# Kernel tuning notes

Measured on AMD Instinct MI355X. Metric: run time of the kernel, lower is better.

Reference implementation:

```python
import jax, jax.numpy as jnp
import numpy as np

N_NODES = 50000
N_EDGES = 800000
IN_F = 128
HID = 256
N_CLS = 10
NUM_GRAPHS = 256


def setup_inputs() -> dict:
    key = jax.random.key(0)
    ks = jax.random.split(key, 8)
    x = jax.random.normal(ks[0], (N_NODES, IN_F), dtype=jnp.float32)
    edge_index = jax.random.randint(ks[1], (2, N_EDGES), 0, N_NODES, dtype=jnp.int64)
    batch = jnp.sort(jax.random.randint(ks[2], (N_NODES,), 0, NUM_GRAPHS, dtype=jnp.int64))
    # Glorot-style init for weights (GCNConv default), zeros bias
    W1 = jax.random.normal(ks[3], (IN_F, HID), dtype=jnp.float32) / np.sqrt(IN_F)
    b1 = jnp.zeros((HID,), dtype=jnp.float32)
    W2 = jax.random.normal(ks[4], (HID, HID), dtype=jnp.float32) / np.sqrt(HID)
    b2 = jnp.zeros((HID,), dtype=jnp.float32)
    Wlin = jax.random.normal(ks[5], (HID, N_CLS), dtype=jnp.float32) / np.sqrt(HID)
    blin = jnp.zeros((N_CLS,), dtype=jnp.float32)
    return {"x": x, "edge_index": edge_index, "batch": batch,
            "W1": W1, "b1": b1, "W2": W2, "b2": b2, "Wlin": Wlin, "blin": blin}


def reference(x, edge_index, batch, W1, b1, W2, b2, Wlin, blin):
    N = x.shape[0]
    # PyG GCNConv default: add self-loops, symmetric normalization D^-1/2 A D^-1/2
    loop = jnp.arange(N, dtype=edge_index.dtype)
    src = jnp.concatenate([edge_index[0], loop])  # message source (row)
    dst = jnp.concatenate([edge_index[1], loop])  # aggregation target (col)
    deg = jax.ops.segment_sum(jnp.ones_like(dst, dtype=x.dtype), dst, num_segments=N)
    dinv = jnp.where(deg > 0, jax.lax.rsqrt(deg), 0.0)
    norm = dinv[src] * dinv[dst]  # [E+N]

    def gcn_conv(h, W, b):
        h = h @ W                          # linear transform first (GCNConv)
        msg = h[src] * norm[:, None]       # gather + edge scale
        agg = jax.ops.segment_sum(msg, dst, num_segments=N)  # scatter-add
        return agg + b

    h = jax.nn.relu(gcn_conv(x, W1, b1))
    h = gcn_conv(h, W2, b2)

    # global_mean_pool over batch ids
    counts = jax.ops.segment_sum(jnp.ones((N,), x.dtype), batch, num_segments=NUM_GRAPHS)
    pooled = jax.ops.segment_sum(h, batch, num_segments=NUM_GRAPHS)
    pooled = pooled / jnp.maximum(counts, 1.0)[:, None]  # [NUM_GRAPHS, HID]

    return pooled @ Wlin + blin  # forward returns logits (softmax unused in forward)
```

## Files before the change

### kernel.cpp

```cpp
#include <hip/hip_runtime.h>
#include <hip/hip_bf16.h>

typedef __hip_bfloat16 bf16;
typedef __attribute__((ext_vector_type(8))) short short8;
typedef __attribute__((ext_vector_type(4))) float f32x4;
typedef __attribute__((ext_vector_type(2))) float f32x2;

#define N_NODES 50000
#define N_EDGES 800000
#define IN_F    128
#define HID     256
#define N_CLS   10
#define N_GRAPH 256

#define NB 98
#define PBLOCKS 256

__device__ __forceinline__ int IG(const int* __restrict__ p, int i, int w) {
    return w ? p[2 * i] : p[i];
}
__device__ __forceinline__ float LF(const void* __restrict__ p, int i, int isbf) {
    return isbf ? __bfloat162float(((const bf16*)p)[i]) : ((const float*)p)[i];
}
__device__ __forceinline__ float b2f(unsigned short h) {
    union { unsigned u; float f; } c; c.u = ((unsigned)h) << 16; return c.f;
}
__device__ __forceinline__ unsigned short f2b(float x) {
    bf16 h = __float2bfloat16(x);
    union { bf16 b; unsigned short u; } c; c.b = h; return c.u;
}
__device__ __forceinline__ float f8s(unsigned b) {
    union { unsigned u; float f; } c;
    c.u = ((b & 0x80u) << 24) | ((b & 0x7Fu) << 20);
    return c.f;
}
#define F8SCALE 0x1p120f
__device__ __forceinline__ unsigned f2fp8(float x) {
    unsigned short h = f2b(x * 0x1p-120f);
    unsigned s = ((unsigned)h >> 8) & 0x80u;
    unsigned mag = (unsigned)h & 0x7FFFu;
    unsigned r = (mag + 7u + ((mag >> 4) & 1u)) >> 4;
    if (r > 0x7Eu) r = 0x7Eu;
    return s | r;
}

#if defined(__has_builtin)
#if __has_builtin(__builtin_amdgcn_cvt_pk_f32_fp8)
#define HW_FP8 1
#endif
#if __has_builtin(__builtin_amdgcn_cvt_pk_fp8_f32)
#define HW_FP8E 1
#endif
#endif

__device__ __forceinline__ f32x2 cvt2lo(unsigned v) {
#ifdef HW_FP8
    return __builtin_amdgcn_cvt_pk_f32_fp8((int)v, false);
#else
    f32x2 r; r[0] = f8s(v & 0xFF) * F8SCALE; r[1] = f8s((v >> 8) & 0xFF) * F8SCALE; return r;
#endif
}
__device__ __forceinline__ f32x2 cvt2hi(unsigned v) {
#ifdef HW_FP8
    return __builtin_amdgcn_cvt_pk_f32_fp8((int)v, true);
#else
    f32x2 r; r[0] = f8s((v >> 16) & 0xFF) * F8SCALE; r[1] = f8s(v >> 24) * F8SCALE; return r;
#endif
}
__device__ __forceinline__ unsigned pk4_fp8(float v0, float v1, float v2, float v3) {
#ifdef HW_FP8E
    int o = __builtin_amdgcn_cvt_pk_fp8_f32(v0, v1, 0, false);
    o = __builtin_amdgcn_cvt_pk_fp8_f32(v2, v3, o, true);
    return (unsigned)o;
#else
    return f2fp8(v0) | (f2fp8(v1) << 8) | (f2fp8(v2) << 16) | (f2fp8(v3) << 24);
#endif
}

__global__ __launch_bounds__(256) void k_partA1(const int* __restrict__ ei, int* __restrict__ bucketCnt,
                                                int* __restrict__ blockBase,
                                                const unsigned short* __restrict__ x,
                                                int* __restrict__ flags, int E, int N) {
    int t = threadIdx.x;
    if (blockIdx.x == PBLOCKS) {
        __shared__ int nz, cnt;
        if (t == 0) { nz = 0; cnt = 0; }
        __syncthreads();
        int found = 0, c = 0;
        for (int s = 0; s < 4; ++s) {
            int idx = 2 * (t * 4 + s) + 1;
            if (ei[idx] != 0) found = 1;
        }
        for (int s = 0; s < 8; ++s) {
            unsigned short h = x[t * 8 + s];
            int e = (h >> 7) & 0xFF;
            if (e >= 110 && e <= 135) c++;
        }
        if (found) atomicAdd(&nz, 1);
        atomicAdd(&cnt, c);
        __syncthreads();
        if (t == 0) {
            flags[0] = (nz == 0) ? 1 : 0;
            flags[1] = (cnt > 1536) ? 1 : 0;
        }
        return;
    }
    __shared__ int h[NB];
    __shared__ int wsh;
    if (t == 0) wsh = 0;
    if (t < NB) h[t] = 0;
    __syncthreads();
    int found = 0;
    for (int s = 0; s < 4; ++s) {
        int idx = 2 * (t * 4 + s) + 1;
        if (ei[idx] != 0) found = 1;
    }
    if (found) atomicAdd(&wsh, 1);
    __syncthreads();
    int w = (wsh == 0) ? 1 : 0;
    for (int e = blockIdx.x * 256 + t; e < E; e += PBLOCKS * 256) {
        int d = IG(ei, E + e, w);
        int s = IG(ei, e, w);
        if ((unsigned)d < (unsigned)N && (unsigned)s < (unsigned)N)
            atomicAdd(&h[d >> 9], 1);
    }
    __syncthreads();
    if (t < NB)
        blockBase[blockIdx.x * NB + t] = atomicAdd(&bucketCnt[t * 16], h[t]);
}

__global__ __launch_bounds__(128) void k_bscan(const int* __restrict__ bucketCnt,
                                               int* __restrict__ bucketBase) {
    __shared__ int s[128];
    int t = threadIdx.x;
    int v = (t < NB) ? bucketCnt[t * 16] : 0;
    s[t] = v;
    __syncthreads();
    for (int off = 1; off < 128; off <<= 1) {
        int add = (t >= off) ? s[t - off] : 0;
        __syncthreads();
        s[t] += add;
        __syncthreads();
    }
    if (t <= NB) bucketBase[t] = (t < NB) ? (s[t] - v) : s[NB - 1] + 0;
    if (t == NB - 1) bucketBase[NB] = s[t];
}

__global__ __launch_bounds__(256) void k_partA2(const int* __restrict__ ei,
                                                const int* __restrict__ bucketBase,
                                                const int* __restrict__ blockBase,
                                                unsigned* __restrict__ part,
                                                const int* __restrict__ flags, int E, int N) {
    __shared__ int cur[NB];
    int t = threadIdx.x;
    if (t < NB) cur[t] = bucketBase[t] + blockBase[blockIdx.x * NB + t];
    __syncthreads();
    int w = flags[0];
    for (int e = blockIdx.x * 256 + t; e < E; e += PBLOCKS * 256) {
        int d = IG(ei, E + e, w);
        int s = IG(ei, e, w);
        if ((unsigned)d < (unsigned)N && (unsigned)s < (unsigned)N) {
            int slot = atomicAdd(&cur[d >> 9], 1);
            part[slot] = ((unsigned)(d & 511) << 16) | (unsigned)s;
        }
    }
}

#define PB_W1 98
#define PB_W2 226
#define PB_GB 482
#define PB_TOT 678
__global__ __launch_bounds__(256) void k_partB(const unsigned* __restrict__ part,
                                               const int* __restrict__ bucketBase,
                                               int* __restrict__ rowptr, float* __restrict__ dinv,
                                               int* __restrict__ col,
                                               const void* __restrict__ W1, unsigned short* __restrict__ w1t,
                                               const void* __restrict__ W2, unsigned short* __restrict__ w2t,
                                               const int* __restrict__ batch, int* __restrict__ gstart,
                                               const int* __restrict__ flags, int N) {
    int b = blockIdx.x, t = threadIdx.x;
    if (b >= NB) {
        int fb = flags[1];
        if (b < PB_W2) {
            int i = (b - PB_W1) * 256 + t;
            int n = i >> 7, k = i & 127;
            w1t[i] = f2b(LF(W1, k * 256 + n, fb));
        } else if (b < PB_GB) {
            int i = (b - PB_W2) * 256 + t;
            int n = i >> 8, k = i & 255;
            w2t[i] = f2b(LF(W2, k * 256 + n, fb));
        } else {
            int i = (b - PB_GB) * 256 + t;
            if (i <= N_NODES) {
                int w = flags[0];
                int prev = (i == 0) ? -1 : IG(batch, i - 1, w);
                int cur  = (i == N_NODES) ? N_GRAPH : IG(batch, i, w);
                if (prev < -1) prev = -1;
                if (cur > N_GRAPH) cur = N_GRAPH;
                for (int g = prev + 1; g <= cur; ++g)
                    if (g >= 0 && g <= N_GRAPH) gstart[g] = i;
            }
        }
        return;
    }
    __shared__ int hist[512];
    __shared__ int scn[512];
    __shared__ int pair[256];
    int s0 = bucketBase[b], e0 = bucketBase[b + 1];
    hist[t] = 0; hist[t + 256] = 0;
    __syncthreads();
    for (int j = s0 + t; j < e0; j += 256)
        atomicAdd(&hist[part[j] >> 16], 1);
    __syncthreads();
    int a0 = hist[2 * t], a1 = hist[2 * t + 1];
    int pv = a0 + a1;
    pair[t] = pv;
    __syncthreads();
    for (int off = 1; off < 256; off <<= 1) {
        int add = (t >= off) ? pair[t - off] : 0;
        __syncthreads();
        pair[t] += add;
        __syncthreads();
    }
    int pbase = pair[t] - pv;
    scn[2 * t] = pbase;
    scn[2 * t + 1] = pbase + a0;
    __syncthreads();
#pragma unroll
    for (int hh = 0; hh < 2; ++hh) {
        int l = t + hh * 256;
        int node = b * 512 + l;
        if (node < N) {
            rowptr[node] = s0 + scn[l];
            dinv[node] = rsqrtf((float)(hist[l] + 1));
        }
    }
    if (b == 0 && t == 0) rowptr[N] = bucketBase[NB];
    __syncthreads();
    for (int j = s0 + t; j < e0; j += 256) {
        unsigned p = part[j];
        int pos = s0 + atomicAdd(&scn[p >> 16], 1);
        col[pos] = (int)(p & 0xFFFFu);
    }
}

#define CVTX_BLOCKS 6250
__global__ __launch_bounds__(256) void k_cvt(const void* __restrict__ x, const float* __restrict__ dinv,
                                             unsigned char* __restrict__ xs8,
                                             const int* __restrict__ flags) {
    int fb = flags[1];
    int gid = blockIdx.x * 256 + threadIdx.x;
    int row = gid >> 5;
    float d = dinv[row];
    float vx, vy, vz, vw;
    if (fb) {
        ushort4 v = ((const ushort4*)x)[gid];
        vx = b2f(v.x); vy = b2f(v.y); vz = b2f(v.z); vw = b2f(v.w);
    } else {
        float4 v = ((const float4*)x)[gid];
        vx = v.x; vy = v.y; vz = v.z; vw = v.w;
    }
    ((unsigned*)xs8)[gid] = pk4_fp8(vx * d, vy * d, vz * d, vw * d);
}

__global__ __launch_bounds__(256) void k_gcn1(const unsigned short* __restrict__ A,
                                              const unsigned short* __restrict__ B1t,
                                              unsigned char* __restrict__ C8, int M,
                                              const float* __restrict__ dinv,
                                              const void* __restrict__ bias1,
                                              const int* __restrict__ flags) {
    __shared__ unsigned short As1[64 * 136];
    int t = threadIdx.x;
    int lane = t & 63;
    int w = t >> 6;
    int bm = blockIdx.x * 64;
    int l15 = lane & 15, quad = lane >> 4;
    int fb = flags[1];

    {
        const uint4* src = (const uint4*)&A[(size_t)bm * 128];
#pragma unroll
        for (int j = 0; j < 4; ++j) {
            int f = t + j * 256;
            int row = f >> 4, cu = f & 15;
            *(uint4*)&As1[row * 136 + cu * 8] = src[(size_t)row * 16 + cu];
        }
    }
    __syncthreads();

    f32x4 acc[4][4];
#pragma unroll
    for (int ar = 0; ar < 4; ++ar)
#pragma unroll
        for (int tt = 0; tt < 4; ++tt) acc[ar][tt] = (f32x4){0.f, 0.f, 0.f, 0.f};

#pragma unroll
    for (int ks = 0; ks < 4; ++ks) {
        short8 a[4], b[4];
#pragma unroll
        for (int ar = 0; ar < 4; ++ar)
            a[ar] = *(const short8*)&As1[(ar * 16 + l15) * 136 + ks * 32 + quad * 8];
#pragma unroll
        for (int tt = 0; tt < 4; ++tt)
            b[tt] = *(const short8*)&B1t[(size_t)(w * 64 + tt * 16 + l15) * 128 + ks * 32 + quad * 8];
#pragma unroll
        for (int tt = 0; tt < 4; ++tt)
#pragma unroll
            for (int ar = 0; ar < 4; ++ar)
                acc[ar][tt] = __builtin_amdgcn_mfma_f32_16x16x32_bf16(b[tt], a[ar], acc[ar][tt], 0, 0, 0);
    }

    float drow[4];
#pragma unroll
    for (int ar = 0; ar < 4; ++ar) {
        int row = bm + ar * 16 + l15;
        drow[ar] = (row < M) ? dinv[row] : 1.f;
    }
    __syncthreads();
    unsigned* Cs = (unsigned*)As1;
#pragma unroll
    for (int tt = 0; tt < 4; ++tt) {
        int colb = w * 64 + tt * 16 + quad * 4;
        float bc[4];
#pragma unroll
        for (int rr = 0; rr < 4; ++rr) bc[rr] = LF(bias1, colb + rr, fb);
#pragma unroll
        for (int ar = 0; ar < 4; ++ar) {
            float v0 = fmaxf(fmaf(acc[ar][tt][0], drow[ar], bc[0]), 0.f) * drow[ar];
            float v1 = fmaxf(fmaf(acc[ar][tt][1], drow[ar], bc[1]), 0.f) * drow[ar];
            float v2 = fmaxf(fmaf(acc[ar][tt][2], drow[ar], bc[2]), 0.f) * drow[ar];
            float v3 = fmaxf(fmaf(acc[ar][tt][3], drow[ar], bc[3]), 0.f) * drow[ar];
            Cs[(ar * 16 + l15) * 68 + w * 16 + tt * 4 + quad] = pk4_fp8(v0, v1, v2, v3);
        }
    }
    __syncthreads();
    int r = t >> 2, h = t & 3;
    if (bm + r < M) {
        const unsigned* src = Cs + r * 68 + h * 16;
        uint4* dst = (uint4*)&C8[(size_t)(bm + r) * 256 + h * 64];
#pragma unroll
        for (int j = 0; j < 4; ++j) dst[j] = *(const uint4*)(src + j * 4);
    }
}

__global__ __launch_bounds__(256) void k_agg2(const unsigned char* __restrict__ XS,
                                              const int* __restrict__ rowptr, const int* __restrict__ col,
                                              unsigned short* __restrict__ Hout, int N) {
    int jb = blockIdx.x;
    int x8 = jb & 7, k = jb >> 3;
    int gIdx = k >> 4, win = k & 15;
    int node0 = (gIdx * 8 + x8) * 64 + win * 4;
    int lane = threadIdx.x & 63;
    int i = node0 + (threadIdx.x >> 6);
    if (i >= N) return;
    int fo = lane * 2;
    unsigned sv = *(const unsigned short*)&XS[(size_t)i * 128 + fo];
    f32x2 a = cvt2lo(sv);
    int s = rowptr[i], e = rowptr[i + 1];
    int j = s;
    while (j + 16 <= e) {
        unsigned v[16];
#pragma unroll
        for (int q = 0; q < 16; ++q)
            v[q] = *(const unsigned short*)&XS[(size_t)col[j + q] * 128 + fo];
#pragma unroll
        for (int q = 0; q < 16; ++q) a += cvt2lo(v[q]);
        j += 16;
    }
    if (j + 8 <= e) {
        unsigned v[8];
#pragma unroll
        for (int q = 0; q < 8; ++q)
            v[q] = *(const unsigned short*)&XS[(size_t)col[j + q] * 128 + fo];
#pragma unroll
        for (int q = 0; q < 8; ++q) a += cvt2lo(v[q]);
        j += 8;
    }
    if (j + 4 <= e) {
        unsigned v[4];
#pragma unroll
        for (int q = 0; q < 4; ++q)
            v[q] = *(const unsigned short*)&XS[(size_t)col[j + q] * 128 + fo];
#pragma unroll
        for (int q = 0; q < 4; ++q) a += cvt2lo(v[q]);
        j += 4;
    }
    for (; j < e; ++j)
        a += cvt2lo(*(const unsigned short*)&XS[(size_t)col[j] * 128 + fo]);
    ushort2 o;
    o.x = f2b(a[0]); o.y = f2b(a[1]);
    *(ushort2*)&Hout[(size_t)i * 128 + fo] = o;
}

__global__ __launch_bounds__(256) void k_agg4p(const unsigned char* __restrict__ XW,
                                               const int* __restrict__ rowptr, const int* __restrict__ col,
                                               const float* __restrict__ dinv,
                                               const int* __restrict__ batch,
                                               const int* __restrict__ flags,
                                               float* __restrict__ partial,
                                               float* __restrict__ pooledX, int N) {
    __shared__ float red[4][256];
    __shared__ int gs[4];
    int t = threadIdx.x;
    int lane = t & 63, sub = t >> 6;
    int i = blockIdx.x * 4 + sub;
    int fo = lane * 4;
    float v[4] = {0.f, 0.f, 0.f, 0.f};
    int g = -1;
    if (i < N) {
        g = IG(batch, i, flags[0]);
        unsigned sv = *(const unsigned*)&XW[(size_t)i * 256 + fo];
        f32x2 a01 = cvt2lo(sv), a23 = cvt2hi(sv);
        int s = rowptr[i], e = rowptr[i + 1];
        int j = s;
        while (j + 16 <= e) {
            unsigned vv[16];
#pragma unroll
            for (int q = 0; q < 16; ++q)
                vv[q] = *(const unsigned*)&XW[(size_t)col[j + q] * 256 + fo];
#pragma unroll
            for (int q = 0; q < 16; ++q) { a01 += cvt2lo(vv[q]); a23 += cvt2hi(vv[q]); }
            j += 16;
        }
        if (j + 8 <= e) {
            unsigned vv[8];
#pragma unroll
            for (int q = 0; q < 8; ++q)
                vv[q] = *(const unsigned*)&XW[(size_t)col[j + q] * 256 + fo];
#pragma unroll
            for (int q = 0; q < 8; ++q) { a01 += cvt2lo(vv[q]); a23 += cvt2hi(vv[q]); }
            j += 8;
        }
        if (j + 4 <= e) {
            unsigned vv[4];
#pragma unroll
            for (int q = 0; q < 4; ++q)
                vv[q] = *(const unsigned*)&XW[(size_t)col[j + q] * 256 + fo];
#pragma unroll
            for (int q = 0; q < 4; ++q) { a01 += cvt2lo(vv[q]); a23 += cvt2hi(vv[q]); }
            j += 4;
        }
        for (; j < e; ++j) {
            unsigned vv = *(const unsigned*)&XW[(size_t)col[j] * 256 + fo];
            a01 += cvt2lo(vv); a23 += cvt2hi(vv);
        }
        float di = dinv[i];
        v[0] = a01[0] * di; v[1] = a01[1] * di;
        v[2] = a23[0] * di; v[3] = a23[1] * di;
    }
    if (lane == 0) gs[sub] = g;
#pragma unroll
    for (int k2 = 0; k2 < 4; ++k2) red[sub][fo + k2] = v[k2];
    __syncthreads();
    bool uni = (gs[0] >= 0) && gs[0] == gs[1] && gs[1] == gs[2] && gs[2] == gs[3];
    if (uni) {
        float s4 = red[0][t] + red[1][t] + red[2][t] + red[3][t];
        partial[(size_t)blockIdx.x * 256 + t] = s4;
    } else if (g >= 0) {
#pragma unroll
        for (int k2 = 0; k2 < 4; ++k2)
            atomicAdd(&pooledX[g * 256 + fo + k2], v[k2]);
    }
}

__global__ __launch_bounds__(512) void k_poolfinal(const float* __restrict__ partial,
                                                   const float* __restrict__ pooledX,
                                                   const int* __restrict__ gstart,
                                                   const unsigned short* __restrict__ w2t,
                                                   const void* __restrict__ b2,
                                                   const void* __restrict__ Wlin,
                                                   const void* __restrict__ blin,
                                                   const int* __restrict__ flags,
                                                   void* __restrict__ outv) {
    __shared__ float red[8][256];
    __shared__ float p[256];
    __shared__ float q[256];
    int g = blockIdx.x, t = threadIdx.x;
    int sub = t >> 6, lane = t & 63;
    int s = gstart[g], e = gstart[g + 1];
    int cnt = e - s;
    int b0 = (s + 3) >> 2, b1 = e >> 2;
    int fo = lane * 4;
    float a0 = 0.f, a1 = 0.f, a2 = 0.f, a3 = 0.f;
    for (int b = b0 + sub; b < b1; b += 8) {
        float4 v = *(const float4*)&partial[(size_t)b * 256 + fo];
        a0 += v.x; a1 += v.y; a2 += v.z; a3 += v.w;
    }
    red[sub][fo + 0] = a0;
    red[sub][fo + 1] = a1;
    red[sub][fo + 2] = a2;
    red[sub][fo + 3] = a3;
    __syncthreads();
    int fb = flags[1];
    if (t < 256) {
        float sum8 = pooledX[g * 256 + t];
#pragma unroll
        for (int qq = 0; qq < 8; ++qq) sum8 += red[qq][t];
        float inv = 1.f / fmaxf((float)cnt, 1.f);
        p[t] = sum8 * inv;
    }
    __syncthreads();
    if (t < 256) {
        float acc2 = (cnt > 0) ? LF(b2, t, fb) : 0.f;
        const unsigned short* wr = &w2t[(size_t)t * 256];
        for (int k = 0; k < 256; k += 8) {
            short8 v8 = *(const short8*)&wr[k];
#pragma unroll
            for (int j = 0; j < 8; ++j)
                acc2 = fmaf(p[k + j], b2f((unsigned short)v8[j]), acc2);
        }
        q[t] = acc2;
    }
    __syncthreads();
    if (t < N_CLS) {
        float sum = LF(blin, t, fb);
        for (int f = 0; f < HID; ++f) sum = fmaf(q[f], LF(Wlin, f * N_CLS + t, fb), sum);
        if (fb) ((bf16*)outv)[g * N_CLS + t] = __float2bfloat16(sum);
        else    ((float*)outv)[g * N_CLS + t] = sum;
    }
}

extern "C" void kernel_launch(void* const* d_in, const int* in_sizes, int n_in,
                              void* d_out, int out_size, void* d_ws, size_t ws_size,
                              hipStream_t stream) {
    (void)n_in; (void)ws_size; (void)in_sizes; (void)out_size;
    const void* x     = d_in[0];
    const int*  ei    = (const int*)d_in[1];
    const int*  batch = (const int*)d_in[2];
    const void* W1    = d_in[3];
    const void* b1    = d_in[4];
    const void* W2    = d_in[5];
    const void* b2    = d_in[6];
    const void* Wl    = d_in[7];
    const void* bl    = d_in[8];

    const int N = N_NODES, E = N_EDGES, F = IN_F, H = HID, G = N_GRAPH;

    char* ws = (char*)d_ws;
    size_t off = 0;
    auto alloc = [&](size_t bytes) -> void* {
        void* p = ws + off;
        off += (bytes + 511) & ~(size_t)511;
        return p;
    };
    unsigned char*  xs8  = (unsigned char*)alloc((size_t)N * F);
    unsigned short* aggX = (unsigned short*)alloc((size_t)N * F * 2);
    unsigned char*  H1s8 = (unsigned char*)alloc((size_t)N * H);
    float*          partial = (float*)alloc((size_t)(N / 4) * H * 4);
    float*          pooledX = (float*)alloc((size_t)G * H * 4);
    unsigned short* w1t  = (unsigned short*)alloc((size_t)H * F * 2);
    unsigned short* w2t  = (unsigned short*)alloc((size_t)H * H * 2);
    int*   bucketCnt = (int*)alloc((size_t)NB * 16 * 4);
    int*   bucketBase = (int*)alloc((size_t)(NB + 1) * 4);
    int*   blockBase = (int*)alloc((size_t)PBLOCKS * NB * 4);
    unsigned* part  = (unsigned*)alloc((size_t)E * 4);
    int*   gstart  = (int*)alloc((size_t)(G + 1) * 4);
    float* dinv    = (float*)alloc((size_t)N * 4);
    int*   rowptr  = (int*)alloc((size_t)(N + 1) * 4);
    int*   flags   = (int*)alloc(512);
    int*   col     = (int*)alloc((size_t)E * 4);
    size_t zero_bytes = (size_t)NB * 16 * 4;

    hipMemsetAsync(bucketCnt, 0, zero_bytes, stream);
    hipMemsetAsync(pooledX, 0, (size_t)G * H * 4, stream);

    k_partA1<<<PBLOCKS + 1, 256, 0, stream>>>(ei, bucketCnt, blockBase,
                                              (const unsigned short*)x, flags, E, N);
    k_bscan<<<1, 128, 0, stream>>>(bucketCnt, bucketBase);
    k_partA2<<<PBLOCKS, 256, 0, stream>>>(ei, bucketBase, blockBase, part, flags, E, N);
    k_partB<<<PB_TOT, 256, 0, stream>>>(part, bucketBase, rowptr, dinv, col,
                                        W1, w1t, W2, w2t, batch, gstart, flags, N);
    k_cvt<<<CVTX_BLOCKS, 256, 0, stream>>>(x, dinv, xs8, flags);

    int g64 = (N + 63) >> 6;
    int aggBlocks = ((g64 + 7) >> 3) * 8 * 16;
    int nbAgg = (N + 3) / 4;

    k_agg2<<<aggBlocks, 256, 0, stream>>>(xs8, rowptr, col, aggX, N);
    k_gcn1<<<g64, 256, 0, stream>>>(aggX, w1t, H1s8, N, dinv, b1, flags);
    k_agg4p<<<nbAgg, 256, 0, stream>>>(H1s8, rowptr, col, dinv, batch, flags, partial, pooledX, N);
    k_poolfinal<<<G, 512, 0, stream>>>(partial, pooledX, gstart, w2t, b2, Wl, bl, flags, d_out);
}
```

Baseline: 242.6 us.

## Fuse edge partition count and scatter into one kernel using fixed-capacity buckets

Merges the two edge-partitioning passes into one kernel. Each thread keeps its 13 edges in registers, counts them into a block histogram, and reserves a block-wide range per bucket with one global atomic. It then scatters packed edges into per-bucket regions of fixed capacity, and partB reads each bucket by its count. This removes one kernel launch, the blockBase array and the second read of edge_index. In exchange, a bucket holding more than CAP edges would overflow, and the partition buffer is sized NB*CAP rather than E.

```diff
diff --git a/kernel.cpp b/kernel.cpp
--- a/kernel.cpp
+++ b/kernel.cpp
@@ -15,6 +15,7 @@
 
 #define NB 98
 #define PBLOCKS 256
+#define CAP 16384
 
 __device__ __forceinline__ int IG(const int* __restrict__ p, int i, int w) {
     return w ? p[2 * i] : p[i];
@@ -77,10 +78,10 @@
 #endif
 }
 
-__global__ __launch_bounds__(256) void k_partA1(const int* __restrict__ ei, int* __restrict__ bucketCnt,
-                                                int* __restrict__ blockBase,
-                                                const unsigned short* __restrict__ x,
-                                                int* __restrict__ flags, int E, int N) {
+__global__ __launch_bounds__(256) void k_part1(const int* __restrict__ ei, int* __restrict__ bucketCnt,
+                                               unsigned* __restrict__ part,
+                                               const unsigned short* __restrict__ x,
+                                               int* __restrict__ flags, int E, int N) {
     int t = threadIdx.x;
     if (blockIdx.x == PBLOCKS) {
         __shared__ int nz, cnt;
@@ -118,15 +119,33 @@
     if (found) atomicAdd(&wsh, 1);
     __syncthreads();
     int w = (wsh == 0) ? 1 : 0;
-    for (int e = blockIdx.x * 256 + t; e < E; e += PBLOCKS * 256) {
-        int d = IG(ei, E + e, w);
-        int s = IG(ei, e, w);
-        if ((unsigned)d < (unsigned)N && (unsigned)s < (unsigned)N)
-            atomicAdd(&h[d >> 9], 1);
-    }
-    __syncthreads();
-    if (t < NB)
-        blockBase[blockIdx.x * NB + t] = atomicAdd(&bucketCnt[t * 16], h[t]);
+    unsigned ed[13];
+#pragma unroll
+    for (int k = 0; k < 13; ++k) {
+        int e = blockIdx.x * 256 + t + k * (PBLOCKS * 256);
+        unsigned val = 0xFFFFFFFFu;
+        if (e < E) {
+            int d = IG(ei, E + e, w);
+            int s = IG(ei, e, w);
+            if ((unsigned)d < (unsigned)N && (unsigned)s < (unsigned)N) {
+                val = ((unsigned)(d >> 9) << 25) | ((unsigned)(d & 511) << 16) | (unsigned)s;
+                atomicAdd(&h[d >> 9], 1);
+            }
+        }
+        ed[k] = val;
+    }
+    __syncthreads();
+    if (t < NB) h[t] = atomicAdd(&bucketCnt[t * 16], h[t]);
+    __syncthreads();
+#pragma unroll
+    for (int k = 0; k < 13; ++k) {
+        unsigned val = ed[k];
+        if (val != 0xFFFFFFFFu) {
+            int bkt = (int)(val >> 25);
+            int slot = atomicAdd(&h[bkt], 1);
+            part[(size_t)bkt * CAP + slot] = val & 0x01FFFFFFu;
+        }
+    }
 }
 
 __global__ __launch_bounds__(128) void k_bscan(const int* __restrict__ bucketCnt,
@@ -146,31 +165,12 @@
     if (t == NB - 1) bucketBase[NB] = s[t];
 }
 
-__global__ __launch_bounds__(256) void k_partA2(const int* __restrict__ ei,
-                                                const int* __restrict__ bucketBase,
-                                                const int* __restrict__ blockBase,
-                                                unsigned* __restrict__ part,
-                                                const int* __restrict__ flags, int E, int N) {
-    __shared__ int cur[NB];
-    int t = threadIdx.x;
-    if (t < NB) cur[t] = bucketBase[t] + blockBase[blockIdx.x * NB + t];
-    __syncthreads();
-    int w = flags[0];
-    for (int e = blockIdx.x * 256 + t; e < E; e += PBLOCKS * 256) {
-        int d = IG(ei, E + e, w);
-        int s = IG(ei, e, w);
-        if ((unsigned)d < (unsigned)N && (unsigned)s < (unsigned)N) {
-            int slot = atomicAdd(&cur[d >> 9], 1);
-            part[slot] = ((unsigned)(d & 511) << 16) | (unsigned)s;
-        }
-    }
-}
-
 #define PB_W1 98
 #define PB_W2 226
 #define PB_GB 482
 #define PB_TOT 678
 __global__ __launch_bounds__(256) void k_partB(const unsigned* __restrict__ part,
+                                               const int* __restrict__ bucketCnt,
                                                const int* __restrict__ bucketBase,
                                                int* __restrict__ rowptr, float* __restrict__ dinv,
                                                int* __restrict__ col,
@@ -206,11 +206,13 @@
     __shared__ int hist[512];
     __shared__ int scn[512];
     __shared__ int pair[256];
-    int s0 = bucketBase[b], e0 = bucketBase[b + 1];
+    size_t s0p = (size_t)b * CAP;
+    int cnt = bucketCnt[b * 16];
+    int s0c = bucketBase[b];
     hist[t] = 0; hist[t + 256] = 0;
     __syncthreads();
-    for (int j = s0 + t; j < e0; j += 256)
-        atomicAdd(&hist[part[j] >> 16], 1);
+    for (int j = t; j < cnt; j += 256)
+        atomicAdd(&hist[part[s0p + j] >> 16], 1);
     __syncthreads();
     int a0 = hist[2 * t], a1 = hist[2 * t + 1];
     int pv = a0 + a1;
@@ -231,15 +233,15 @@
         int l = t + hh * 256;
         int node = b * 512 + l;
         if (node < N) {
-            rowptr[node] = s0 + scn[l];
+            rowptr[node] = s0c + scn[l];
             dinv[node] = rsqrtf((float)(hist[l] + 1));
         }
     }
     if (b == 0 && t == 0) rowptr[N] = bucketBase[NB];
     __syncthreads();
-    for (int j = s0 + t; j < e0; j += 256) {
-        unsigned p = part[j];
-        int pos = s0 + atomicAdd(&scn[p >> 16], 1);
+    for (int j = t; j < cnt; j += 256) {
+        unsigned p = part[s0p + j];
+        int pos = s0c + atomicAdd(&scn[p >> 16], 1);
         col[pos] = (int)(p & 0xFFFFu);
     }
 }
@@ -552,8 +554,7 @@
     unsigned short* w2t  = (unsigned short*)alloc((size_t)H * H * 2);
     int*   bucketCnt = (int*)alloc((size_t)NB * 16 * 4);
     int*   bucketBase = (int*)alloc((size_t)(NB + 1) * 4);
-    int*   blockBase = (int*)alloc((size_t)PBLOCKS * NB * 4);
-    unsigned* part  = (unsigned*)alloc((size_t)E * 4);
+    unsigned* part  = (unsigned*)alloc((size_t)NB * CAP * 4);
     int*   gstart  = (int*)alloc((size_t)(G + 1) * 4);
     float* dinv    = (float*)alloc((size_t)N * 4);
     int*   rowptr  = (int*)alloc((size_t)(N + 1) * 4);
@@ -564,11 +565,10 @@
     hipMemsetAsync(bucketCnt, 0, zero_bytes, stream);
     hipMemsetAsync(pooledX, 0, (size_t)G * H * 4, stream);
 
-    k_partA1<<<PBLOCKS + 1, 256, 0, stream>>>(ei, bucketCnt, blockBase,
-                                              (const unsigned short*)x, flags, E, N);
+    k_part1<<<PBLOCKS + 1, 256, 0, stream>>>(ei, bucketCnt, part,
+                                             (const unsigned short*)x, flags, E, N);
     k_bscan<<<1, 128, 0, stream>>>(bucketCnt, bucketBase);
-    k_partA2<<<PBLOCKS, 256, 0, stream>>>(ei, bucketBase, blockBase, part, flags, E, N);
-    k_partB<<<PB_TOT, 256, 0, stream>>>(part, bucketBase, rowptr, dinv, col,
+    k_partB<<<PB_TOT, 256, 0, stream>>>(part, bucketCnt, bucketBase, rowptr, dinv, col,
                                         W1, w1t, W2, w2t, batch, gstart, flags, N);
     k_cvt<<<CVTX_BLOCKS, 256, 0, stream>>>(x, dinv, xs8, flags);
 
```

After: 237.7 us (median of 2 runs). -2.0%, faster.
